# Kernel tuning notes

Measured on AMD Instinct MI355X. Metric: run time of the kernel, lower is better.

The kernel has to match this reference:

```python
import jax, jax.numpy as jnp
import numpy as np

N = 2048


def setup_inputs() -> dict:
    key = jax.random.key(0)
    k1, k2 = jax.random.split(key)
    graph1 = jax.random.uniform(k1, (N, N), dtype=jnp.float32)
    graph2 = jax.random.uniform(k2, (N, N), dtype=jnp.float32)
    return {"graph1": graph1, "graph2": graph2}


def _degree_dist(adj):
    return adj.sum(axis=-1)


def _clustering(adj):
    # diag(A @ A @ A) computed without materializing the full cube:
    # tri_i = sum_j (A@A)_{ij} * A_{ji}
    a2 = adj @ adj                      # [n, n]
    tri = (a2 * adj.T).sum(axis=-1)     # [n]
    deg = adj.sum(axis=-1)
    deg = jnp.where(deg < 2, 1.0, deg)  # torch: deg[deg < 2] = 1
    return tri / (deg * (deg - 1.0))


def reference(graph1, graph2):
    d1 = _degree_dist(graph1)
    d2 = _degree_dist(graph2)
    degree_sim = jnp.exp(-jnp.abs(d1 - d2).mean())
    c1 = _clustering(graph1)
    c2 = _clustering(graph2)
    cluster_sim = jnp.exp(-jnp.abs(c1 - c2).mean())
    overall = (degree_sim + cluster_sim) / 2.0
    return (degree_sim, cluster_sim, overall)
```

## Files before the change

kernel.cpp:

```cpp
#include <hip/hip_runtime.h>

#define NN 2048

typedef unsigned short u16;
typedef __attribute__((ext_vector_type(8))) short short8;
typedef __attribute__((ext_vector_type(4))) float floatx4;

__device__ __forceinline__ u16 f2bf(float f) {
  unsigned u = __float_as_uint(f);
  u += 0x7FFF + ((u >> 16) & 1);
  return (u16)(u >> 16);
}

__device__ __forceinline__ float bf2f(u16 h) {
  return __uint_as_float(((unsigned)h) << 16);
}

__device__ __forceinline__ void load_lds16(const u16* g, u16* l) {
  __builtin_amdgcn_global_load_lds(
      (const __attribute__((address_space(1))) unsigned int*)g,
      (__attribute__((address_space(3))) unsigned int*)l,
      16, 0, 0);
}

__global__ __launch_bounds__(256) void prep_kernel(
    const float* __restrict__ A1, const float* __restrict__ A2,
    u16* __restrict__ Abf, u16* __restrict__ AbfT,
    float* __restrict__ degp, float* __restrict__ tri) {
  __shared__ u16 Tl[64 * 17 * 4];
  const int bx = blockIdx.x, by = blockIdx.y, bz = blockIdx.z;
  const float* __restrict__ A = bz ? A2 : A1;
  u16* __restrict__ ab = Abf + (size_t)bz * (NN * (size_t)NN);
  u16* __restrict__ at = AbfT + (size_t)bz * (NN * (size_t)NN);
  float* __restrict__ dp = degp + (size_t)bz * (32 * NN);
  const int t = threadIdx.x;
  const int r0 = by * 64, c0 = bx * 64;
  const int q = t >> 4, cs = t & 15;

  if (bx == 0 && t < 64) tri[bz * NN + by * 64 + t] = 0.f;

  u16 m[4][4];
#pragma unroll
  for (int d = 0; d < 4; ++d) {
    const int r = 4 * q + d;
    const float4 fv = *(const float4*)(A + (size_t)(r0 + r) * NN + c0 + cs * 4);
    ushort4 b;
    b.x = f2bf(fv.x); b.y = f2bf(fv.y); b.z = f2bf(fv.z); b.w = f2bf(fv.w);
    *(ushort4*)(ab + (size_t)(r0 + r) * NN + c0 + cs * 4) = b;
    m[d][0] = b.x; m[d][1] = b.y; m[d][2] = b.z; m[d][3] = b.w;
    float s = fv.x + fv.y + fv.z + fv.w;
    s += __shfl_xor(s, 1); s += __shfl_xor(s, 2);
    s += __shfl_xor(s, 4); s += __shfl_xor(s, 8);
    if (cs == 0) dp[(size_t)(r0 + r) * 32 + bx] = s;
  }
#pragma unroll
  for (int e = 0; e < 4; ++e) {
    ushort4 tc;
    tc.x = m[0][e]; tc.y = m[1][e]; tc.z = m[2][e]; tc.w = m[3][e];
    *(ushort4*)(Tl + ((4 * cs + e) * 17 + q) * 4) = tc;
  }
  __syncthreads();
#pragma unroll
  for (int p = 0; p < 2; ++p) {
    const int rp = p * 32 + (t >> 3);
    const int mm = t & 7;
    const ushort4 v0 = *(const ushort4*)(Tl + (rp * 17 + 2 * mm) * 4);
    const ushort4 v1 = *(const ushort4*)(Tl + (rp * 17 + 2 * mm + 1) * 4);
    ushort4* dst = (ushort4*)(at + (size_t)(c0 + rp) * NN + r0 + mm * 8);
    dst[0] = v0;
    dst[1] = v1;
  }
}

#define MFMA_BODY(PB)                                                     \
  {                                                                       \
    short8 af[4], bfr[4];                                                 \
    _Pragma("unroll")                                                     \
    for (int tm = 0; tm < 4; ++tm)                                        \
      af[tm] = *(const short8*)(smem + (PB) + aoff[tm]);                  \
    _Pragma("unroll")                                                     \
    for (int tn = 0; tn < 4; ++tn)                                        \
      bfr[tn] = *(const short8*)(smem + (PB) + boff[tn]);                 \
    _Pragma("unroll")                                                     \
    for (int tm = 0; tm < 4; ++tm)                                        \
      _Pragma("unroll")                                                   \
      for (int tn = 0; tn < 4; ++tn)                                      \
        acc[tm][tn] = __builtin_amdgcn_mfma_f32_16x16x32_bf16(            \
            af[tm], bfr[tn], acc[tm][tn], 0, 0, 0);                       \
  }

#define PREFETCH(KK, DB)                                                  \
  load_lds16(gA0 + (KK), smem + (DB) + sA0);                              \
  load_lds16(gA1 + (KK), smem + (DB) + sA1);                              \
  load_lds16(gB0 + (KK), smem + (DB) + sB0);                              \
  load_lds16(gB1 + (KK), smem + (DB) + sB1);

#define FENCE asm volatile("" ::: "memory")

__global__ __launch_bounds__(256, 4) void gemm_tri_kernel(
    const u16* __restrict__ Abf, const u16* __restrict__ AbfT,
    float* __restrict__ tri) {
  __shared__ u16 smem[17408];

  const int tid = threadIdx.x;
  const int w = tid >> 6, lane = tid & 63;
  const int wm = w >> 1, wn = w & 1;
  const int cl = lane & 15, g = lane >> 4;
  const int i0 = blockIdx.y * 128, j0 = blockIdx.x * 128;
  const int mz = blockIdx.z >> 1, kz = blockIdx.z & 1;
  const size_t mat = (size_t)mz * (NN * (size_t)NN);
  const u16* __restrict__ Am = Abf + mat;
  const u16* __restrict__ ATm = AbfT + mat;
  float* __restrict__ triM = tri + mz * NN;

  const int s0 = (w * 2 + 0) * 64 + lane;
  const int s1 = (w * 2 + 1) * 64 + lane;
  const int r0s = s0 >> 2, c0s = (s0 & 3) ^ ((r0s >> 1) & 3);
  const int r1s = s1 >> 2, c1s = (s1 & 3) ^ ((r1s >> 1) & 3);
  const int kbase = kz * 1024;
  const u16* gA0 = Am + (size_t)(i0 + r0s) * NN + kbase + c0s * 8;
  const u16* gA1 = Am + (size_t)(i0 + r1s) * NN + kbase + c1s * 8;
  const u16* gB0 = ATm + (size_t)(j0 + r0s) * NN + kbase + c0s * 8;
  const u16* gB1 = ATm + (size_t)(j0 + r1s) * NN + kbase + c1s * 8;
  const int sA0 = (w * 2 + 0) * 512, sA1 = (w * 2 + 1) * 512;
  const int sB0 = 4096 + sA0, sB1 = 4096 + sA1;

  const int swz = g ^ ((cl >> 1) & 3);
  int aoff[4], boff[4];
#pragma unroll
  for (int tm = 0; tm < 4; ++tm)
    aoff[tm] = (wm * 64 + tm * 16 + cl) * 32 + swz * 8;
#pragma unroll
  for (int tn = 0; tn < 4; ++tn)
    boff[tn] = 4096 + (wn * 64 + tn * 16 + cl) * 32 + swz * 8;

  floatx4 acc[4][4] = {};

  PREFETCH(0, 0)

#pragma unroll 1
  for (int d = 0; d < 15; ++d) {
    FENCE; __builtin_amdgcn_s_barrier(); FENCE;
    PREFETCH((2 * d + 1) * 32, 8192)
    __builtin_amdgcn_s_waitcnt(0x0F74);
    FENCE; __builtin_amdgcn_s_barrier(); FENCE;
    MFMA_BODY(0)
    FENCE; __builtin_amdgcn_s_barrier(); FENCE;
    PREFETCH((2 * d + 2) * 32, 0)
    __builtin_amdgcn_s_waitcnt(0x0F74);
    FENCE; __builtin_amdgcn_s_barrier(); FENCE;
    MFMA_BODY(8192)
  }
  FENCE; __builtin_amdgcn_s_barrier(); FENCE;
  PREFETCH(31 * 32, 8192)
  __builtin_amdgcn_s_waitcnt(0x0F74);
  FENCE; __builtin_amdgcn_s_barrier(); FENCE;
  MFMA_BODY(0)
  FENCE; __builtin_amdgcn_s_barrier(); FENCE;
  __builtin_amdgcn_s_waitcnt(0x0F70);
  FENCE; __builtin_amdgcn_s_barrier(); FENCE;
  MFMA_BODY(8192)

  __syncthreads();
#pragma unroll
  for (int it = 0; it < 8; ++it) {
    const int idx = tid + it * 256;
    const int r = idx >> 4, co = (idx & 15) * 8;
    *(uint4*)(smem + r * 136 + co) =
        *(const uint4*)(ATm + (size_t)(i0 + r) * NN + j0 + co);
  }
  __syncthreads();

#pragma unroll
  for (int tm = 0; tm < 4; ++tm) {
#pragma unroll
    for (int reg = 0; reg < 4; ++reg) {
      const int rloc = wm * 64 + tm * 16 + g * 4 + reg;
      float v = 0.f;
#pragma unroll
      for (int tn = 0; tn < 4; ++tn) {
        const int cloc = wn * 64 + tn * 16 + cl;
        v += acc[tm][tn][reg] * bf2f(smem[rloc * 136 + cloc]);
      }
      v += __shfl_xor(v, 1);
      v += __shfl_xor(v, 2);
      v += __shfl_xor(v, 4);
      v += __shfl_xor(v, 8);
      if (cl == 0) atomicAdd(&triM[i0 + rloc], v);
    }
  }
}

__global__ __launch_bounds__(1024) void finalize1_kernel(
    const float* __restrict__ degp, const float* __restrict__ tri,
    float* __restrict__ part) {
  __shared__ float red[32];
  const int t = threadIdx.x;
  const int r = blockIdx.x * 128 + (t >> 3);
  const int q = (t & 7) * 4;
  const float4 v1 = *(const float4*)(degp + (size_t)r * 32 + q);
  const float4 v2 = *(const float4*)(degp + 32 * NN + (size_t)r * 32 + q);
  float d1 = v1.x + v1.y + v1.z + v1.w;
  float d2 = v2.x + v2.y + v2.z + v2.w;
#pragma unroll
  for (int m = 1; m < 8; m <<= 1) {
    d1 += __shfl_xor(d1, m);
    d2 += __shfl_xor(d2, m);
  }
  float sdd = 0.f, scc = 0.f;
  if ((t & 7) == 0) {
    const float t1 = tri[r], t2 = tri[NN + r];
    const float e1 = d1 < 2.f ? 1.f : d1;
    const float e2 = d2 < 2.f ? 1.f : d2;
    sdd = fabsf(d1 - d2);
    scc = fabsf(t1 / (e1 * (e1 - 1.f)) - t2 / (e2 * (e2 - 1.f)));
  }
#pragma unroll
  for (int m = 8; m < 64; m <<= 1) {
    sdd += __shfl_xor(sdd, m);
    scc += __shfl_xor(scc, m);
  }
  const int wv = t >> 6, ln = t & 63;
  if (ln == 0) { red[wv] = sdd; red[16 + wv] = scc; }
  __syncthreads();
  if (t == 0) {
    float a = 0.f, b = 0.f;
#pragma unroll
    for (int i = 0; i < 16; ++i) { a += red[i]; b += red[16 + i]; }
    part[blockIdx.x * 2 + 0] = a;
    part[blockIdx.x * 2 + 1] = b;
  }
}

__global__ void finalize2_kernel(const float* __restrict__ part,
                                 float* __restrict__ out) {
  if (threadIdx.x == 0) {
    float a = 0.f, b = 0.f;
#pragma unroll
    for (int i = 0; i < 16; ++i) { a += part[i * 2]; b += part[i * 2 + 1]; }
    const float ds = expf(-a * (1.f / (float)NN));
    const float cs = expf(-b * (1.f / (float)NN));
    out[0] = ds;
    out[1] = cs;
    out[2] = 0.5f * (ds + cs);
  }
}

extern "C" void kernel_launch(void* const* d_in, const int* in_sizes, int n_in,
                              void* d_out, int out_size, void* d_ws, size_t ws_size,
                              hipStream_t stream) {
  (void)in_sizes; (void)n_in; (void)out_size; (void)ws_size;
  const float* A1 = (const float*)d_in[0];
  const float* A2 = (const float*)d_in[1];
  float* out = (float*)d_out;

  u16* Abf = (u16*)d_ws;
  u16* AbfT = Abf + 2 * (size_t)NN * NN;
  float* tri = (float*)(AbfT + 2 * (size_t)NN * NN);
  float* degp = tri + 2 * NN;
  float* part = degp + 2 * 32 * NN;

  prep_kernel<<<dim3(32, 32, 2), 256, 0, stream>>>(A1, A2, Abf, AbfT, degp, tri);
  gemm_tri_kernel<<<dim3(16, 16, 4), 256, 0, stream>>>(Abf, AbfT, tri);
  finalize1_kernel<<<16, 1024, 0, stream>>>(degp, tri, part);
  finalize2_kernel<<<1, 64, 0, stream>>>(part, out);
}
```

Measured before the change: 128.8 us.

## Switch A@A GEMM operands from bf16 to fp8 e4m3 with fp8 MFMA

The prep kernel now quantizes the adjacency matrices and their transposes to fp8 (e4m3) instead of bf16, which halves the bytes written and later re-read by the GEMM. The GEMM stages 64-byte K chunks per row in LDS with a new swizzle and issues two fp8 16x16x32 MFMAs per tile pair, so it runs half as many K iterations. The epilogue decodes fp8 A^T values in software. The cost is a much coarser operand precision (3 mantissa bits), which may push the clustering sums past the accuracy tolerance.

Result: faster. 115.7 us (-10.2%).

```diff
diff --git a/kernel.cpp b/kernel.cpp
--- a/kernel.cpp
+++ b/kernel.cpp
@@ -3,20 +3,17 @@
 #define NN 2048
 
 typedef unsigned short u16;
-typedef __attribute__((ext_vector_type(8))) short short8;
+typedef unsigned char u8;
 typedef __attribute__((ext_vector_type(4))) float floatx4;
 
-__device__ __forceinline__ u16 f2bf(float f) {
-  unsigned u = __float_as_uint(f);
-  u += 0x7FFF + ((u >> 16) & 1);
-  return (u16)(u >> 16);
-}
-
-__device__ __forceinline__ float bf2f(u16 h) {
-  return __uint_as_float(((unsigned)h) << 16);
-}
-
-__device__ __forceinline__ void load_lds16(const u16* g, u16* l) {
+__device__ __forceinline__ float fp8_to_f32(unsigned v) {
+  const unsigned e = (v >> 3) & 15, m = v & 7;
+  const float norm = __uint_as_float(((e + 120u) << 23) | (m << 20));
+  const float sub = (float)m * 0.001953125f;
+  return e == 0 ? sub : norm;
+}
+
+__device__ __forceinline__ void load_lds16(const u8* g, u8* l) {
   __builtin_amdgcn_global_load_lds(
       (const __attribute__((address_space(1))) unsigned int*)g,
       (__attribute__((address_space(3))) unsigned int*)l,
@@ -25,13 +22,13 @@
 
 __global__ __launch_bounds__(256) void prep_kernel(
     const float* __restrict__ A1, const float* __restrict__ A2,
-    u16* __restrict__ Abf, u16* __restrict__ AbfT,
+    u8* __restrict__ A8, u8* __restrict__ A8T,
     float* __restrict__ degp, float* __restrict__ tri) {
-  __shared__ u16 Tl[64 * 17 * 4];
+  __shared__ unsigned Tl[64 * 17];
   const int bx = blockIdx.x, by = blockIdx.y, bz = blockIdx.z;
   const float* __restrict__ A = bz ? A2 : A1;
-  u16* __restrict__ ab = Abf + (size_t)bz * (NN * (size_t)NN);
-  u16* __restrict__ at = AbfT + (size_t)bz * (NN * (size_t)NN);
+  u8* __restrict__ ab = A8 + (size_t)bz * (NN * (size_t)NN);
+  u8* __restrict__ at = A8T + (size_t)bz * (NN * (size_t)NN);
   float* __restrict__ dp = degp + (size_t)bz * (32 * NN);
   const int t = threadIdx.x;
   const int r0 = by * 64, c0 = bx * 64;
@@ -39,15 +36,15 @@
 
   if (bx == 0 && t < 64) tri[bz * NN + by * 64 + t] = 0.f;
 
-  u16 m[4][4];
+  unsigned rowpack[4];
 #pragma unroll
   for (int d = 0; d < 4; ++d) {
     const int r = 4 * q + d;
     const float4 fv = *(const float4*)(A + (size_t)(r0 + r) * NN + c0 + cs * 4);
-    ushort4 b;
-    b.x = f2bf(fv.x); b.y = f2bf(fv.y); b.z = f2bf(fv.z); b.w = f2bf(fv.w);
-    *(ushort4*)(ab + (size_t)(r0 + r) * NN + c0 + cs * 4) = b;
-    m[d][0] = b.x; m[d][1] = b.y; m[d][2] = b.z; m[d][3] = b.w;
+    int pk = __builtin_amdgcn_cvt_pk_fp8_f32(fv.x, fv.y, 0, false);
+    pk = __builtin_amdgcn_cvt_pk_fp8_f32(fv.z, fv.w, pk, true);
+    rowpack[d] = (unsigned)pk;
+    *(unsigned*)(ab + (size_t)(r0 + r) * NN + c0 + cs * 4) = (unsigned)pk;
     float s = fv.x + fv.y + fv.z + fv.w;
     s += __shfl_xor(s, 1); s += __shfl_xor(s, 2);
     s += __shfl_xor(s, 4); s += __shfl_xor(s, 8);
@@ -55,52 +52,60 @@
   }
 #pragma unroll
   for (int e = 0; e < 4; ++e) {
-    ushort4 tc;
-    tc.x = m[0][e]; tc.y = m[1][e]; tc.z = m[2][e]; tc.w = m[3][e];
-    *(ushort4*)(Tl + ((4 * cs + e) * 17 + q) * 4) = tc;
+    const unsigned tc = ((rowpack[0] >> (8 * e)) & 0xFFu) |
+                        (((rowpack[1] >> (8 * e)) & 0xFFu) << 8) |
+                        (((rowpack[2] >> (8 * e)) & 0xFFu) << 16) |
+                        (((rowpack[3] >> (8 * e)) & 0xFFu) << 24);
+    Tl[(4 * cs + e) * 17 + q] = tc;
   }
   __syncthreads();
 #pragma unroll
   for (int p = 0; p < 2; ++p) {
     const int rp = p * 32 + (t >> 3);
     const int mm = t & 7;
-    const ushort4 v0 = *(const ushort4*)(Tl + (rp * 17 + 2 * mm) * 4);
-    const ushort4 v1 = *(const ushort4*)(Tl + (rp * 17 + 2 * mm + 1) * 4);
-    ushort4* dst = (ushort4*)(at + (size_t)(c0 + rp) * NN + r0 + mm * 8);
-    dst[0] = v0;
-    dst[1] = v1;
-  }
-}
-
-#define MFMA_BODY(PB)                                                     \
-  {                                                                       \
-    short8 af[4], bfr[4];                                                 \
-    _Pragma("unroll")                                                     \
-    for (int tm = 0; tm < 4; ++tm)                                        \
-      af[tm] = *(const short8*)(smem + (PB) + aoff[tm]);                  \
-    _Pragma("unroll")                                                     \
-    for (int tn = 0; tn < 4; ++tn)                                        \
-      bfr[tn] = *(const short8*)(smem + (PB) + boff[tn]);                 \
-    _Pragma("unroll")                                                     \
-    for (int tm = 0; tm < 4; ++tm)                                        \
-      _Pragma("unroll")                                                   \
-      for (int tn = 0; tn < 4; ++tn)                                      \
-        acc[tm][tn] = __builtin_amdgcn_mfma_f32_16x16x32_bf16(            \
-            af[tm], bfr[tn], acc[tm][tn], 0, 0, 0);                       \
-  }
-
-#define PREFETCH(KK, DB)                                                  \
-  load_lds16(gA0 + (KK), smem + (DB) + sA0);                              \
-  load_lds16(gA1 + (KK), smem + (DB) + sA1);                              \
-  load_lds16(gB0 + (KK), smem + (DB) + sB0);                              \
+    uint2 v;
+    v.x = Tl[rp * 17 + 2 * mm];
+    v.y = Tl[rp * 17 + 2 * mm + 1];
+    *(uint2*)(at + (size_t)(c0 + rp) * NN + r0 + mm * 8) = v;
+  }
+}
+
+#define MFMA_BODY(PB)                                                      \
+  {                                                                        \
+    long aL[4][2], bL[4][2];                                               \
+    _Pragma("unroll")                                                      \
+    for (int tm = 0; tm < 4; ++tm) {                                       \
+      aL[tm][0] = *(const long*)(smem + (PB) + aoff[tm][0]);               \
+      aL[tm][1] = *(const long*)(smem + (PB) + aoff[tm][1]);               \
+    }                                                                      \
+    _Pragma("unroll")                                                      \
+    for (int tn = 0; tn < 4; ++tn) {                                       \
+      bL[tn][0] = *(const long*)(smem + (PB) + boff[tn][0]);               \
+      bL[tn][1] = *(const long*)(smem + (PB) + boff[tn][1]);               \
+    }                                                                      \
+    _Pragma("unroll")                                                      \
+    for (int tm = 0; tm < 4; ++tm)                                         \
+      _Pragma("unroll")                                                    \
+      for (int tn = 0; tn < 4; ++tn) {                                     \
+        acc[tm][tn] = __builtin_amdgcn_mfma_f32_16x16x32_fp8_fp8(          \
+            aL[tm][0], bL[tn][0], acc[tm][tn], 0, 0, 0);                   \
+        acc[tm][tn] = __builtin_amdgcn_mfma_f32_16x16x32_fp8_fp8(          \
+            aL[tm][1], bL[tn][1], acc[tm][tn], 0, 0, 0);                   \
+      }                                                                    \
+  }
+
+#define PREFETCH(KK, DB)                                                   \
+  load_lds16(gA0 + (KK), smem + (DB) + sA0);                               \
+  load_lds16(gA1 + (KK), smem + (DB) + sA1);                               \
+  load_lds16(gB0 + (KK), smem + (DB) + sB0);                               \
   load_lds16(gB1 + (KK), smem + (DB) + sB1);
 
 #define FENCE asm volatile("" ::: "memory")
 
 __global__ __launch_bounds__(256, 4) void gemm_tri_kernel(
-    const u16* __restrict__ Abf, const u16* __restrict__ AbfT,
+    const u8* __restrict__ A8, const u8* __restrict__ A8T,
     float* __restrict__ tri) {
-  __shared__ u16 smem[17408];
+  __shared__ __align__(16) u8 smem[32768];
 
   const int tid = threadIdx.x;
   const int w = tid >> 6, lane = tid & 63;
@@ -109,8 +114,8 @@
   const int i0 = blockIdx.y * 128, j0 = blockIdx.x * 128;
   const int mz = blockIdx.z >> 1, kz = blockIdx.z & 1;
   const size_t mat = (size_t)mz * (NN * (size_t)NN);
-  const u16* __restrict__ Am = Abf + mat;
-  const u16* __restrict__ ATm = AbfT + mat;
+  const u8* __restrict__ Am = A8 + mat;
+  const u8* __restrict__ ATm = A8T + mat;
   float* __restrict__ triM = tri + mz * NN;
 
   const int s0 = (w * 2 + 0) * 64 + lane;
@@ -118,55 +123,64 @@
   const int r0s = s0 >> 2, c0s = (s0 & 3) ^ ((r0s >> 1) & 3);
   const int r1s = s1 >> 2, c1s = (s1 & 3) ^ ((r1s >> 1) & 3);
   const int kbase = kz * 1024;
-  const u16* gA0 = Am + (size_t)(i0 + r0s) * NN + kbase + c0s * 8;
-  const u16* gA1 = Am + (size_t)(i0 + r1s) * NN + kbase + c1s * 8;
-  const u16* gB0 = ATm + (size_t)(j0 + r0s) * NN + kbase + c0s * 8;
-  const u16* gB1 = ATm + (size_t)(j0 + r1s) * NN + kbase + c1s * 8;
-  const int sA0 = (w * 2 + 0) * 512, sA1 = (w * 2 + 1) * 512;
-  const int sB0 = 4096 + sA0, sB1 = 4096 + sA1;
-
-  const int swz = g ^ ((cl >> 1) & 3);
-  int aoff[4], boff[4];
-#pragma unroll
-  for (int tm = 0; tm < 4; ++tm)
-    aoff[tm] = (wm * 64 + tm * 16 + cl) * 32 + swz * 8;
-#pragma unroll
-  for (int tn = 0; tn < 4; ++tn)
-    boff[tn] = 4096 + (wn * 64 + tn * 16 + cl) * 32 + swz * 8;
+  const u8* gA0 = Am + (size_t)(i0 + r0s) * NN + kbase + c0s * 16;
+  const u8* gA1 = Am + (size_t)(i0 + r1s) * NN + kbase + c1s * 16;
+  const u8* gB0 = ATm + (size_t)(j0 + r0s) * NN + kbase + c0s * 16;
+  const u8* gB1 = ATm + (size_t)(j0 + r1s) * NN + kbase + c1s * 16;
+  const int sA0 = (w * 2 + 0) * 1024, sA1 = (w * 2 + 1) * 1024;
+  const int sB0 = 8192 + sA0, sB1 = 8192 + sA1;
+
+  const int rsw = (cl >> 1) & 3;
+  const int sub = (g & 1) * 8, ch = g >> 1;
+  int aoff[4][2], boff[4][2];
+#pragma unroll
+  for (int tm = 0; tm < 4; ++tm) {
+    const int r = wm * 64 + tm * 16 + cl;
+#pragma unroll
+    for (int h = 0; h < 2; ++h)
+      aoff[tm][h] = r * 64 + (((2 * h + ch) ^ rsw) * 16) + sub;
+  }
+#pragma unroll
+  for (int tn = 0; tn < 4; ++tn) {
+    const int r = wn * 64 + tn * 16 + cl;
+#pragma unroll
+    for (int h = 0; h < 2; ++h)
+      boff[tn][h] = 8192 + r * 64 + (((2 * h + ch) ^ rsw) * 16) + sub;
+  }
 
   floatx4 acc[4][4] = {};
 
   PREFETCH(0, 0)
 
 #pragma unroll 1
-  for (int d = 0; d < 15; ++d) {
-    FENCE; __builtin_amdgcn_s_barrier(); FENCE;
-    PREFETCH((2 * d + 1) * 32, 8192)
+  for (int d = 0; d < 7; ++d) {
+    FENCE; __builtin_amdgcn_s_barrier(); FENCE;
+    PREFETCH((2 * d + 1) * 64, 16384)
     __builtin_amdgcn_s_waitcnt(0x0F74);
     FENCE; __builtin_amdgcn_s_barrier(); FENCE;
     MFMA_BODY(0)
     FENCE; __builtin_amdgcn_s_barrier(); FENCE;
-    PREFETCH((2 * d + 2) * 32, 0)
+    PREFETCH((2 * d + 2) * 64, 0)
     __builtin_amdgcn_s_waitcnt(0x0F74);
     FENCE; __builtin_amdgcn_s_barrier(); FENCE;
-    MFMA_BODY(8192)
-  }
-  FENCE; __builtin_amdgcn_s_barrier(); FENCE;
-  PREFETCH(31 * 32, 8192)
+    MFMA_BODY(16384)
+  }
+  FENCE; __builtin_amdgcn_s_barrier(); FENCE;
+  PREFETCH(15 * 64, 16384)
   __builtin_amdgcn_s_waitcnt(0x0F74);
   FENCE; __builtin_amdgcn_s_barrier(); FENCE;
   MFMA_BODY(0)
   FENCE; __builtin_amdgcn_s_barrier(); FENCE;
   __builtin_amdgcn_s_waitcnt(0x0F70);
   FENCE; __builtin_amdgcn_s_barrier(); FENCE;
-  MFMA_BODY(8192)
-
-  __syncthreads();
-#pragma unroll
-  for (int it = 0; it < 8; ++it) {
+  MFMA_BODY(16384)
+
+  __syncthreads();
+#pragma unroll
+  for (int it = 0; it < 4; ++it) {
     const int idx = tid + it * 256;
-    const int r = idx >> 4, co = (idx & 15) * 8;
-    *(uint4*)(smem + r * 136 + co) =
+    const int r = idx >> 3, co = (idx & 7) * 16;
+    *(uint4*)(smem + r * 144 + co) =
         *(const uint4*)(ATm + (size_t)(i0 + r) * NN + j0 + co);
   }
   __syncthreads();
@@ -180,7 +194,7 @@
 #pragma unroll
       for (int tn = 0; tn < 4; ++tn) {
         const int cloc = wn * 64 + tn * 16 + cl;
-        v += acc[tm][tn][reg] * bf2f(smem[rloc * 136 + cloc]);
+        v += acc[tm][tn][reg] * fp8_to_f32(smem[rloc * 144 + cloc]);
       }
       v += __shfl_xor(v, 1);
       v += __shfl_xor(v, 2);
@@ -254,14 +268,14 @@
   const float* A2 = (const float*)d_in[1];
   float* out = (float*)d_out;
 
-  u16* Abf = (u16*)d_ws;
-  u16* AbfT = Abf + 2 * (size_t)NN * NN;
-  float* tri = (float*)(AbfT + 2 * (size_t)NN * NN);
+  u8* A8 = (u8*)d_ws;
+  u8* A8T = A8 + 2 * (size_t)NN * NN;
+  float* tri = (float*)(A8T + 2 * (size_t)NN * NN);
   float* degp = tri + 2 * NN;
   float* part = degp + 2 * 32 * NN;
 
-  prep_kernel<<<dim3(32, 32, 2), 256, 0, stream>>>(A1, A2, Abf, AbfT, degp, tri);
-  gemm_tri_kernel<<<dim3(16, 16, 4), 256, 0, stream>>>(Abf, AbfT, tri);
+  prep_kernel<<<dim3(32, 32, 2), 256, 0, stream>>>(A1, A2, A8, A8T, degp, tri);
+  gemm_tri_kernel<<<dim3(16, 16, 4), 256, 0, stream>>>(A8, A8T, tri);
   finalize1_kernel<<<16, 1024, 0, stream>>>(degp, tri, part);
   finalize2_kernel<<<1, 64, 0, stream>>>(part, out);
 }
```
